# Kernel tuning notes

Hardware: AMD Instinct MI355X
Metric: run time of the kernel (lower is better)

Reference implementation:

```python
import jax, jax.numpy as jnp
import numpy as np

COPY = 4
PAD = 0
EPS = 1e-10


def setup_inputs() -> dict:
    key = jax.random.key(0)
    k1, k2, k3, k4, k5, k6 = jax.random.split(key, 6)
    B, S, H, V, SRC_V = 1024, 128, 1024, 50000, 50000
    hidden = jax.random.normal(k1, (B, H), dtype=jnp.float32)
    src = jax.random.randint(k2, (B, S), 0, SRC_V, dtype=jnp.int64)
    attn = jax.random.uniform(k3, (B, S), dtype=jnp.float32)
    W = jax.random.normal(k4, (V, H), dtype=jnp.float32) * 0.02
    b = jax.random.normal(k5, (V,), dtype=jnp.float32) * 0.02
    alignment = jax.random.randint(k6, (SRC_V,), 0, V, dtype=jnp.int64)
    return {"hidden": hidden, "src": src, "attn": attn, "W": W, "b": b, "alignment": alignment}


def reference(hidden, src, attn, W, b, alignment):
    # logits = Linear(hidden): [B, V]
    logits = jnp.einsum("bh,vh->bv", hidden, W) + b
    # zero-out (set to 1e-10) the COPY logit before softmax
    mod_logits = logits.at[:, COPY].set(1e-10)
    prob = jax.nn.softmax(mod_logits, axis=-1)                      # [B, V]
    copy = jax.nn.sigmoid(logits[:, COPY])[:, None]                 # [B, 1]
    mul_attn = attn * copy                                          # [B, S]
    prob = prob * (1.0 - copy)                                      # [B, V]
    # map source token ids to target vocab ids, then batched scatter-add
    tgt_idx = alignment[src]                                        # [B, S]
    B = prob.shape[0]
    rows = jnp.arange(B)[:, None]                                   # [B, 1]
    out_prob = prob.at[rows, tgt_idx].add(mul_attn)                 # fused batched index_add
    out_prob = out_prob.at[:, PAD].set(EPS)
    norm = out_prob.sum(axis=1, keepdims=True)
    return jnp.log(out_prob / norm + EPS)
```

## Files before the change

kernel.cpp:

```cpp
#include <hip/hip_runtime.h>

#define B_   1024
#define S_   128
#define H_   1024
#define V_   50000
#define EPSF 1e-10f

typedef float f32x4 __attribute__((ext_vector_type(4)));
typedef short s16x8 __attribute__((ext_vector_type(8)));

__device__ __forceinline__ void gload_lds16(const void* g, void* l) {
  __builtin_amdgcn_global_load_lds(
      (const __attribute__((address_space(1))) void*)g,
      (__attribute__((address_space(3))) void*)l, 16, 0, 0);
}

__device__ __forceinline__ void split8(f32x4 a, f32x4 b, s16x8& hi, s16x8& lo) {
  float x[8] = {a[0], a[1], a[2], a[3], b[0], b[1], b[2], b[3]};
#pragma unroll
  for (int j = 0; j < 8; ++j) {
    unsigned u = __float_as_uint(x[j]);
    hi[j] = (short)(u >> 16);
    float hf = __uint_as_float(u & 0xFFFF0000u);
    float l  = x[j] - hf;
    lo[j] = (short)(__float_as_uint(l) >> 16);
  }
}

constexpr int NBN = (V_ + 127) / 128;

__global__ __launch_bounds__(256, 2) void gemm_logits(
    const float* __restrict__ hid, const float* __restrict__ W,
    const float* __restrict__ bias, float* __restrict__ out) {
  __shared__ float ldsA[2][128 * 32];
  __shared__ float ldsB[2][128 * 32];

  int bid = blockIdx.x;
  int xcd = bid & 7;
  int t8  = bid >> 3;
  int mb  = t8 & 7;
  int nbg = t8 >> 3;
  int nb  = nbg * 8 + xcd;
  if (nb >= NBN) return;

  const int brow = mb * 128;
  const int bcol = nb * 128;
  const int tid  = threadIdx.x;
  const int lane = tid & 63;
  const int wid  = tid >> 6;
  const int wr   = wid >> 1;
  const int wc   = wid & 1;

  const float* gA[4];
  const float* gB[4];
#pragma unroll
  for (int i = 0; i < 4; ++i) {
    int row = i * 32 + (tid >> 3);
    int g   = (tid & 7) ^ (row & 7);
    gA[i] = hid + (size_t)(brow + row) * H_ + g * 4;
    int gv = bcol + row;
    if (gv > V_ - 1) gv = V_ - 1;
    gB[i] = W + (size_t)gv * H_ + g * 4;
  }

  auto stage = [&](int bufi, int k0) {
#pragma unroll
    for (int i = 0; i < 4; ++i)
      gload_lds16(gA[i] + k0, (char*)(&ldsA[bufi][0]) + i * 4096 + wid * 1024);
#pragma unroll
    for (int i = 0; i < 4; ++i)
      gload_lds16(gB[i] + k0, (char*)(&ldsB[bufi][0]) + i * 4096 + wid * 1024);
  };

  const int kg  = lane >> 4;
  const int r15 = lane & 15;
  int offA0[4], offA1[4], offB0[4], offB1[4];
#pragma unroll
  for (int i = 0; i < 4; ++i) {
    int ra = wr * 64 + i * 16 + r15;
    int wa = ra & 7;
    offA0[i] = ra * 128 + ((((kg << 1) | 0) ^ wa) << 4);
    offA1[i] = ra * 128 + ((((kg << 1) | 1) ^ wa) << 4);
    int rb = wc * 64 + i * 16 + r15;
    int wb = rb & 7;
    offB0[i] = rb * 128 + ((((kg << 1) | 0) ^ wb) << 4);
    offB1[i] = rb * 128 + ((((kg << 1) | 1) ^ wb) << 4);
  }

  f32x4 acc[4][4];
#pragma unroll
  for (int i = 0; i < 4; ++i)
#pragma unroll
    for (int j = 0; j < 4; ++j) acc[i][j] = (f32x4){0.f, 0.f, 0.f, 0.f};

  stage(0, 0);
  __syncthreads();
  int buf = 0;
#pragma unroll 1
  for (int t = 0; t < 32; ++t) {
    if (t < 31) stage(buf ^ 1, (t + 1) * 32);
    const char* bA = (const char*)(&ldsA[buf][0]);
    const char* bB = (const char*)(&ldsB[buf][0]);
    s16x8 ah[4], al[4], bh[4], bl[4];
#pragma unroll
    for (int mi = 0; mi < 4; ++mi)
      split8(*(const f32x4*)(bA + offA0[mi]), *(const f32x4*)(bA + offA1[mi]),
             ah[mi], al[mi]);
#pragma unroll
    for (int ni = 0; ni < 4; ++ni)
      split8(*(const f32x4*)(bB + offB0[ni]), *(const f32x4*)(bB + offB1[ni]),
             bh[ni], bl[ni]);
#pragma unroll
    for (int mi = 0; mi < 4; ++mi)
#pragma unroll
      for (int ni = 0; ni < 4; ++ni) {
        acc[mi][ni] = __builtin_amdgcn_mfma_f32_16x16x32_bf16(ah[mi], bh[ni], acc[mi][ni], 0, 0, 0);
        acc[mi][ni] = __builtin_amdgcn_mfma_f32_16x16x32_bf16(ah[mi], bl[ni], acc[mi][ni], 0, 0, 0);
        acc[mi][ni] = __builtin_amdgcn_mfma_f32_16x16x32_bf16(al[mi], bh[ni], acc[mi][ni], 0, 0, 0);
      }
    __syncthreads();
    buf ^= 1;
  }

  const int colbase = bcol + wc * 64 + r15;
  const int rowbase = brow + wr * 64 + ((lane >> 4) << 2);
#pragma unroll
  for (int ni = 0; ni < 4; ++ni) {
    int col = colbase + ni * 16;
    if (col < V_) {
      float bv = bias[col];
#pragma unroll
      for (int mi = 0; mi < 4; ++mi) {
        int row0 = rowbase + mi * 16;
#pragma unroll
        for (int j = 0; j < 4; ++j)
          out[(size_t)(row0 + j) * V_ + col] = acc[mi][ni][j] + bv;
      }
    }
  }
}

__global__ __launch_bounds__(256) void row_finish(
    float* __restrict__ out, const float* __restrict__ attn,
    const int* __restrict__ src, const int* __restrict__ algn) {
  __shared__ float sRed[4];
  __shared__ float sBro[4];
  __shared__ float sSt[4];
  __shared__ float sVal[S_];
  __shared__ int   sTgt[S_];
  __shared__ int   rTgt[S_];
  __shared__ float rVal[S_];
  __shared__ float rLog[S_];

  const int b = blockIdx.x;
  const int tid = threadIdx.x;
  const int lane = tid & 63, wid = tid >> 6;
  float* row = out + (size_t)b * V_;

  float z = 0.f;
  for (int c = tid; c < V_ / 4; c += 256) {
    f32x4 f = ((const f32x4*)row)[c];
    z += __expf(f[0]) + __expf(f[1]) + __expf(f[2]) + __expf(f[3]);
  }
#pragma unroll
  for (int off = 32; off; off >>= 1) z += __shfl_down(z, off);
  if (lane == 0) sRed[wid] = z;
  if (tid == 0) sBro[2] = 0.f;
  __syncthreads();
  if (tid == 0) {
    float Zr = sRed[0] + sRed[1] + sRed[2] + sRed[3];
    float l4 = row[4];
    sBro[0] = Zr - __expf(l4) + __expf(EPSF);
    sBro[1] = 1.f / (1.f + __expf(-l4));
  }
  __syncthreads();
  const float Z = sBro[0], cp = sBro[1];

  if (tid < S_) {
    int sv = src[b * S_ + tid];
    sTgt[tid] = algn[sv];
    sVal[tid] = attn[b * S_ + tid] * cp;
  }
  __syncthreads();
  float sumv = 0.f;
  if (tid < S_) {
    int tgt = sTgt[tid];
    bool first = true;
    float total = 0.f;
    for (int s2 = 0; s2 < S_; ++s2) {
      bool eq = (sTgt[s2] == tgt);
      if (eq && s2 < tid) first = false;
      if (eq) total += sVal[s2];
    }
    if (first && tgt != 0) {
      rTgt[tid] = tgt;
      rVal[tid] = total;
      rLog[tid] = row[tgt];
    } else {
      rTgt[tid] = -1;
    }
    if (first && tgt == 0) sBro[2] = total;
    sumv = sVal[tid];
  }
#pragma unroll
  for (int off = 32; off; off >>= 1) sumv += __shfl_down(sumv, off);
  if (lane == 0) sRed[wid] = sumv;
  __syncthreads();

  if (tid == 0) {
    float sumval = sRed[0] + sRed[1] + sRed[2] + sRed[3];
    float scat0  = sBro[2];
    float p0     = __expf(row[0]) / Z;
    float omc    = 1.f - cp;
    float norm   = omc + sumval + EPSF - p0 * omc - scat0;
    sSt[0] = omc / (Z * norm);
    sSt[1] = __logf(EPSF / norm + EPSF);
    sSt[2] = 1.f / norm;
  }
  __syncthreads();
  const float st0 = sSt[0], st1 = sSt[1], invn = sSt[2];

  for (int c = tid; c < V_ / 4; c += 256) {
    f32x4 f = ((const f32x4*)row)[c];
    int vb  = c * 4;
    f32x4 r;
#pragma unroll
    for (int j = 0; j < 4; ++j) {
      float x = f[j];
      int v   = vb + j;
      if (v == 4) x = EPSF;
      float y = __logf(__expf(x) * st0 + EPSF);
      if (v == 0) y = st1;
      r[j] = y;
    }
    ((f32x4*)row)[c] = r;
  }
  __syncthreads();

  if (tid < S_) {
    int t = rTgt[tid];
    if (t >= 0) {
      float x = (t == 4) ? EPSF : rLog[tid];
      row[t] = __logf(__expf(x) * st0 + invn * rVal[tid] + EPSF);
    }
  }
}

extern "C" void kernel_launch(void* const* d_in, const int* in_sizes, int n_in,
                              void* d_out, int out_size, void* d_ws,
                              size_t ws_size, hipStream_t stream) {
  const float* hid  = (const float*)d_in[0];
  const int*   src  = (const int*)d_in[1];
  const float* attn = (const float*)d_in[2];
  const float* W    = (const float*)d_in[3];
  const float* bias = (const float*)d_in[4];
  const int*   algn = (const int*)d_in[5];
  float* out = (float*)d_out;
  (void)in_sizes; (void)n_in; (void)out_size; (void)d_ws; (void)ws_size;

  gemm_logits<<<dim3(3136), dim3(256), 0, stream>>>(hid, W, bias, out);
  row_finish<<<dim3(B_), dim3(256), 0, stream>>>(out, attn, src, algn);
}
```

Before: 800.8 us.

## Pre-split fp32 operands into bf16 hi/lo planes and fuse softmax sum into GEMM

Adds a pre-pass that splits W and hidden into separate bf16 hi and lo planes in workspace. The GEMM then loads bf16 directly instead of re-splitting fp32 tiles inside the inner loop. The GEMM epilogue also accumulates per-row exp sums through atomics, which removes the first full-row read pass. The row finish is split into a stats kernel, a grid-wide transform and a scatter fixup. The cost is an extra read and write of all of W (about 200MB) on every call, plus more kernel launches. It falls back to the old path when the workspace is too small.

Measured after the change: 783.1 us. 1.02x faster.

```diff
diff --git a/kernel.cpp b/kernel.cpp
--- a/kernel.cpp
+++ b/kernel.cpp
@@ -8,6 +8,18 @@
 
 typedef float f32x4 __attribute__((ext_vector_type(4)));
 typedef short s16x8 __attribute__((ext_vector_type(8)));
+typedef short s16x4 __attribute__((ext_vector_type(4)));
+
+#define OFF_WHI 0ULL
+#define OFF_WLO 102400000ULL
+#define OFF_AHI 204800000ULL
+#define OFF_ALO 206897152ULL
+#define OFF_Z   208994304ULL
+#define OFF_ST  208998400ULL
+#define OFF_RT  209014784ULL
+#define OFF_RV  209539072ULL
+#define OFF_RL  210063360ULL
+#define WS_NEED 210587648ULL
 
 __device__ __forceinline__ void gload_lds16(const void* g, void* l) {
   __builtin_amdgcn_global_load_lds(
@@ -27,13 +39,34 @@
   }
 }
 
+__global__ __launch_bounds__(256) void split_planes(
+    const float* __restrict__ in, short* __restrict__ hi,
+    short* __restrict__ lo, int n4) {
+  for (int g = blockIdx.x * 256 + threadIdx.x; g < n4; g += gridDim.x * 256) {
+    f32x4 x = ((const f32x4*)in)[g];
+    s16x4 h, l;
+#pragma unroll
+    for (int j = 0; j < 4; ++j) {
+      unsigned u = __float_as_uint(x[j]);
+      h[j] = (short)(u >> 16);
+      float hf = __uint_as_float(u & 0xFFFF0000u);
+      l[j] = (short)(__float_as_uint(x[j] - hf) >> 16);
+    }
+    ((s16x4*)hi)[g] = h;
+    ((s16x4*)lo)[g] = l;
+  }
+}
+
+__global__ void zeroZ(float* Z) { Z[blockIdx.x * 256 + threadIdx.x] = 0.f; }
+
 constexpr int NBN = (V_ + 127) / 128;
 
-__global__ __launch_bounds__(256, 2) void gemm_logits(
-    const float* __restrict__ hid, const float* __restrict__ W,
-    const float* __restrict__ bias, float* __restrict__ out) {
-  __shared__ float ldsA[2][128 * 32];
-  __shared__ float ldsB[2][128 * 32];
+__global__ __launch_bounds__(256, 2) void gemm_ps(
+    const short* __restrict__ Whi, const short* __restrict__ Wlo,
+    const short* __restrict__ Ahi, const short* __restrict__ Alo,
+    const float* __restrict__ bias, float* __restrict__ out,
+    float* __restrict__ Z) {
+  __shared__ short lds[2][4][128 * 32];
 
   int bid = blockIdx.x;
   int xcd = bid & 7;
@@ -51,6 +84,238 @@
   const int wr   = wid >> 1;
   const int wc   = wid & 1;
 
+  const int rt0 = wid * 16 + (lane >> 2);
+  const int kc8 = (lane & 3) * 8;
+  const short* pAhi = Ahi + (size_t)(brow + rt0) * H_ + kc8;
+  const short* pAlo = Alo + (size_t)(brow + rt0) * H_ + kc8;
+  int gv0 = bcol + rt0;        if (gv0 > V_ - 1) gv0 = V_ - 1;
+  int gv1 = bcol + 64 + rt0;   if (gv1 > V_ - 1) gv1 = V_ - 1;
+  const short* pBhi0 = Whi + (size_t)gv0 * H_ + kc8;
+  const short* pBhi1 = Whi + (size_t)gv1 * H_ + kc8;
+  const short* pBlo0 = Wlo + (size_t)gv0 * H_ + kc8;
+  const short* pBlo1 = Wlo + (size_t)gv1 * H_ + kc8;
+
+  auto stage = [&](int bufi, int k0) {
+    short* base = &lds[bufi][0][0];
+    gload_lds16(pAhi + k0,          base +               wid * 512);
+    gload_lds16(pAhi + 65536 + k0,  base + 2048 +        wid * 512);
+    gload_lds16(pAlo + k0,          base + 4096 +        wid * 512);
+    gload_lds16(pAlo + 65536 + k0,  base + 4096 + 2048 + wid * 512);
+    gload_lds16(pBhi0 + k0,         base + 8192 +        wid * 512);
+    gload_lds16(pBhi1 + k0,         base + 8192 + 2048 + wid * 512);
+    gload_lds16(pBlo0 + k0,         base + 12288 +       wid * 512);
+    gload_lds16(pBlo1 + k0,         base + 12288 + 2048 + wid * 512);
+  };
+
+  const int kg  = lane >> 4;
+  const int r15 = lane & 15;
+  const int arow = wr * 64 + r15;
+  const int brw  = wc * 64 + r15;
+  const int kofs = kg * 8;
+
+  f32x4 acc[4][4];
+#pragma unroll
+  for (int i = 0; i < 4; ++i)
+#pragma unroll
+    for (int j = 0; j < 4; ++j) acc[i][j] = (f32x4){0.f, 0.f, 0.f, 0.f};
+
+  stage(0, 0);
+  __syncthreads();
+  int buf = 0;
+#pragma unroll 1
+  for (int t = 0; t < 32; ++t) {
+    if (t < 31) stage(buf ^ 1, (t + 1) * 32);
+    const short* bp = &lds[buf][0][0];
+    s16x8 ah[4], al[4], bh[4], bl[4];
+#pragma unroll
+    for (int mi = 0; mi < 4; ++mi) {
+      ah[mi] = *(const s16x8*)(bp + (arow + mi * 16) * 32 + kofs);
+      al[mi] = *(const s16x8*)(bp + 4096 + (arow + mi * 16) * 32 + kofs);
+    }
+#pragma unroll
+    for (int ni = 0; ni < 4; ++ni) {
+      bh[ni] = *(const s16x8*)(bp + 8192 + (brw + ni * 16) * 32 + kofs);
+      bl[ni] = *(const s16x8*)(bp + 12288 + (brw + ni * 16) * 32 + kofs);
+    }
+#pragma unroll
+    for (int mi = 0; mi < 4; ++mi)
+#pragma unroll
+      for (int ni = 0; ni < 4; ++ni)
+        acc[mi][ni] = __builtin_amdgcn_mfma_f32_16x16x32_bf16(ah[mi], bh[ni], acc[mi][ni], 0, 0, 0);
+#pragma unroll
+    for (int mi = 0; mi < 4; ++mi)
+#pragma unroll
+      for (int ni = 0; ni < 4; ++ni)
+        acc[mi][ni] = __builtin_amdgcn_mfma_f32_16x16x32_bf16(ah[mi], bl[ni], acc[mi][ni], 0, 0, 0);
+#pragma unroll
+    for (int mi = 0; mi < 4; ++mi)
+#pragma unroll
+      for (int ni = 0; ni < 4; ++ni)
+        acc[mi][ni] = __builtin_amdgcn_mfma_f32_16x16x32_bf16(al[mi], bh[ni], acc[mi][ni], 0, 0, 0);
+    __syncthreads();
+    buf ^= 1;
+  }
+
+  const int colbase = bcol + wc * 64 + r15;
+  const int rowbase = brow + wr * 64 + ((lane >> 4) << 2);
+  float bv[4];
+  bool  cv[4];
+#pragma unroll
+  for (int ni = 0; ni < 4; ++ni) {
+    int col = colbase + ni * 16;
+    cv[ni] = (col < V_);
+    bv[ni] = bias[cv[ni] ? col : (V_ - 1)];
+  }
+#pragma unroll
+  for (int ni = 0; ni < 4; ++ni) {
+    if (cv[ni]) {
+      int col = colbase + ni * 16;
+#pragma unroll
+      for (int mi = 0; mi < 4; ++mi) {
+        int row0 = rowbase + mi * 16;
+#pragma unroll
+        for (int j = 0; j < 4; ++j)
+          out[(size_t)(row0 + j) * V_ + col] = acc[mi][ni][j] + bv[ni];
+      }
+    }
+  }
+#pragma unroll
+  for (int mi = 0; mi < 4; ++mi) {
+#pragma unroll
+    for (int j = 0; j < 4; ++j) {
+      float s = 0.f;
+#pragma unroll
+      for (int ni = 0; ni < 4; ++ni)
+        if (cv[ni]) s += __expf(acc[mi][ni][j] + bv[ni]);
+      s += __shfl_xor(s, 1);
+      s += __shfl_xor(s, 2);
+      s += __shfl_xor(s, 4);
+      s += __shfl_xor(s, 8);
+      if (r15 == 0) atomicAdd(&Z[rowbase + mi * 16 + j], s);
+    }
+  }
+}
+
+__global__ __launch_bounds__(128) void stats_k(
+    const float* __restrict__ out, const float* __restrict__ attn,
+    const int* __restrict__ src, const int* __restrict__ algn,
+    const float* __restrict__ Z, f32x4* __restrict__ stats,
+    int* __restrict__ rec_tgt, float* __restrict__ rec_val,
+    float* __restrict__ rec_logit) {
+  __shared__ float sVal[S_];
+  __shared__ int   sTgt[S_];
+  __shared__ float sRed[2];
+  __shared__ float sScat0;
+
+  const int b = blockIdx.x;
+  const int tid = threadIdx.x;
+  const int lane = tid & 63, wid = tid >> 6;
+  const float* row = out + (size_t)b * V_;
+
+  if (tid == 0) sScat0 = 0.f;
+  const float l4 = row[4];
+  const float cp = 1.f / (1.f + __expf(-l4));
+  {
+    int sv = src[b * S_ + tid];
+    sTgt[tid] = algn[sv];
+    sVal[tid] = attn[b * S_ + tid] * cp;
+  }
+  __syncthreads();
+  int tgt = sTgt[tid];
+  bool first = true;
+  float total = 0.f;
+  for (int s2 = 0; s2 < S_; ++s2) {
+    bool eq = (sTgt[s2] == tgt);
+    if (eq && s2 < tid) first = false;
+    if (eq) total += sVal[s2];
+  }
+  int o = b * S_ + tid;
+  if (first && tgt != 0) {
+    rec_tgt[o]   = tgt;
+    rec_val[o]   = total;
+    rec_logit[o] = row[tgt];
+  } else {
+    rec_tgt[o] = -1;
+  }
+  if (first && tgt == 0) sScat0 = total;
+
+  float sumv = sVal[tid];
+#pragma unroll
+  for (int off = 32; off; off >>= 1) sumv += __shfl_down(sumv, off);
+  if (lane == 0) sRed[wid] = sumv;
+  __syncthreads();
+  if (tid == 0) {
+    float sumval = sRed[0] + sRed[1];
+    float Zmod   = Z[b] - __expf(l4) + __expf(EPSF);
+    float p0     = __expf(row[0]) / Zmod;
+    float omc    = 1.f - cp;
+    float norm   = omc + sumval + EPSF - p0 * omc - sScat0;
+    f32x4 st;
+    st[0] = omc / (Zmod * norm);
+    st[1] = __logf(EPSF / norm + EPSF);
+    st[2] = 1.f / norm;
+    st[3] = 0.f;
+    stats[b] = st;
+  }
+}
+
+__global__ __launch_bounds__(256) void transform_k(
+    float* __restrict__ out, const f32x4* __restrict__ stats) {
+  const int total = (B_ * (V_ / 4));
+  const int gpr   = V_ / 4;
+  for (int g = blockIdx.x * 256 + threadIdx.x; g < total;
+       g += gridDim.x * 256) {
+    int row = g / gpr;
+    int cg  = g - row * gpr;
+    f32x4 st = stats[row];
+    f32x4 f  = ((const f32x4*)out)[g];
+    int vb   = cg * 4;
+    f32x4 r;
+#pragma unroll
+    for (int j = 0; j < 4; ++j) {
+      float x = f[j];
+      int v   = vb + j;
+      if (v == 4) x = EPSF;
+      float y = __logf(__expf(x) * st[0] + EPSF);
+      if (v == 0) y = st[1];
+      r[j] = y;
+    }
+    ((f32x4*)out)[g] = r;
+  }
+}
+
+__global__ __launch_bounds__(128) void fixup_k(
+    float* __restrict__ out, const f32x4* __restrict__ stats,
+    const int* __restrict__ rec_tgt, const float* __restrict__ rec_val,
+    const float* __restrict__ rec_logit) {
+  int b = blockIdx.x, s = threadIdx.x;
+  int o = b * S_ + s;
+  int t = rec_tgt[o];
+  if (t < 0) return;
+  f32x4 st = stats[b];
+  float x  = (t == 4) ? EPSF : rec_logit[o];
+  out[(size_t)b * V_ + t] = __logf(__expf(x) * st[0] + st[2] * rec_val[o] + EPSF);
+}
+
+__global__ __launch_bounds__(256, 2) void gemm_fb(
+    const float* __restrict__ hid, const float* __restrict__ W,
+    const float* __restrict__ bias, float* __restrict__ out) {
+  __shared__ float ldsA[2][128 * 32];
+  __shared__ float ldsB[2][128 * 32];
+  int bid = blockIdx.x;
+  int xcd = bid & 7;
+  int t8  = bid >> 3;
+  int mb  = t8 & 7;
+  int nbg = t8 >> 3;
+  int nb  = nbg * 8 + xcd;
+  if (nb >= NBN) return;
+  const int brow = mb * 128;
+  const int bcol = nb * 128;
+  const int tid  = threadIdx.x;
+  const int lane = tid & 63;
+  const int wid  = tid >> 6;
+  const int wr   = wid >> 1;
+  const int wc   = wid & 1;
   const float* gA[4];
   const float* gB[4];
 #pragma unroll
@@ -62,7 +327,6 @@
     if (gv > V_ - 1) gv = V_ - 1;
     gB[i] = W + (size_t)gv * H_ + g * 4;
   }
-
   auto stage = [&](int bufi, int k0) {
 #pragma unroll
     for (int i = 0; i < 4; ++i)
@@ -71,7 +335,6 @@
     for (int i = 0; i < 4; ++i)
       gload_lds16(gB[i] + k0, (char*)(&ldsB[bufi][0]) + i * 4096 + wid * 1024);
   };
-
   const int kg  = lane >> 4;
   const int r15 = lane & 15;
   int offA0[4], offA1[4], offB0[4], offB1[4];
@@ -86,13 +349,11 @@
     offB0[i] = rb * 128 + ((((kg << 1) | 0) ^ wb) << 4);
     offB1[i] = rb * 128 + ((((kg << 1) | 1) ^ wb) << 4);
   }
-
   f32x4 acc[4][4];
 #pragma unroll
   for (int i = 0; i < 4; ++i)
 #pragma unroll
     for (int j = 0; j < 4; ++j) acc[i][j] = (f32x4){0.f, 0.f, 0.f, 0.f};
-
   stage(0, 0);
   __syncthreads();
   int buf = 0;
@@ -121,7 +382,6 @@
     __syncthreads();
     buf ^= 1;
   }
-
   const int colbase = bcol + wc * 64 + r15;
   const int rowbase = brow + wr * 64 + ((lane >> 4) << 2);
 #pragma unroll
@@ -151,12 +411,10 @@
   __shared__ int   rTgt[S_];
   __shared__ float rVal[S_];
   __shared__ float rLog[S_];
-
   const int b = blockIdx.x;
   const int tid = threadIdx.x;
   const int lane = tid & 63, wid = tid >> 6;
   float* row = out + (size_t)b * V_;
-
   float z = 0.f;
   for (int c = tid; c < V_ / 4; c += 256) {
     f32x4 f = ((const f32x4*)row)[c];
@@ -175,7 +433,6 @@
   }
   __syncthreads();
   const float Z = sBro[0], cp = sBro[1];
-
   if (tid < S_) {
     int sv = src[b * S_ + tid];
     sTgt[tid] = algn[sv];
@@ -206,7 +463,6 @@
   for (int off = 32; off; off >>= 1) sumv += __shfl_down(sumv, off);
   if (lane == 0) sRed[wid] = sumv;
   __syncthreads();
-
   if (tid == 0) {
     float sumval = sRed[0] + sRed[1] + sRed[2] + sRed[3];
     float scat0  = sBro[2];
@@ -219,7 +475,6 @@
   }
   __syncthreads();
   const float st0 = sSt[0], st1 = sSt[1], invn = sSt[2];
-
   for (int c = tid; c < V_ / 4; c += 256) {
     f32x4 f = ((const f32x4*)row)[c];
     int vb  = c * 4;
@@ -236,7 +491,6 @@
     ((f32x4*)row)[c] = r;
   }
   __syncthreads();
-
   if (tid < S_) {
     int t = rTgt[tid];
     if (t >= 0) {
@@ -256,8 +510,29 @@
   const float* bias = (const float*)d_in[4];
   const int*   algn = (const int*)d_in[5];
   float* out = (float*)d_out;
-  (void)in_sizes; (void)n_in; (void)out_size; (void)d_ws; (void)ws_size;
-
-  gemm_logits<<<dim3(3136), dim3(256), 0, stream>>>(hid, W, bias, out);
-  row_finish<<<dim3(B_), dim3(256), 0, stream>>>(out, attn, src, algn);
-}
+  (void)in_sizes; (void)n_in; (void)out_size;
+
+  if (ws_size >= WS_NEED) {
+    char* ws = (char*)d_ws;
+    short* Whi = (short*)(ws + OFF_WHI);
+    short* Wlo = (short*)(ws + OFF_WLO);
+    short* Ahi = (short*)(ws + OFF_AHI);
+    short* Alo = (short*)(ws + OFF_ALO);
+    float* Z   = (float*)(ws + OFF_Z);
+    f32x4* st  = (f32x4*)(ws + OFF_ST);
+    int*   rt  = (int*)(ws + OFF_RT);
+    float* rv  = (float*)(ws + OFF_RV);
+    float* rl  = (float*)(ws + OFF_RL);
+
+    split_planes<<<dim3(2048), dim3(256), 0, stream>>>(W, Whi, Wlo, V_ * H_ / 4);
+    split_planes<<<dim3(256), dim3(256), 0, stream>>>(hid, Ahi, Alo, B_ * H_ / 4);
+    zeroZ<<<dim3(4), dim3(256), 0, stream>>>(Z);
+    gemm_ps<<<dim3(3136), dim3(256), 0, stream>>>(Whi, Wlo, Ahi, Alo, bias, out, Z);
+    stats_k<<<dim3(B_), dim3(S_), 0, stream>>>(out, attn, src, algn, Z, st, rt, rv, rl);
+    transform_k<<<dim3(2048), dim3(256), 0, stream>>>(out, st);
+    fixup_k<<<dim3(B_), dim3(S_), 0, stream>>>(out, st, rt, rv, rl);
+  } else {
+    gemm_fb<<<dim3(3136), dim3(256), 0, stream>>>(hid, W, bias, out);
+    row_finish<<<dim3(B_), dim3(256), 0, stream>>>(out, attn, src, algn);
+  }
+}
```
